# Optimization experiments

Hardware: AMD Instinct MI355X
Metric: run time of the kernel (lower is better)

## Reference

```python
import jax, jax.numpy as jnp
from jax import lax
import numpy as np

# dims
B, P, M = 256, 192, 321
HIDC, HIDR, HIDS = 128, 128, 8
CK, SKIP, HW = 6, 24, 24
SCI_K = 5
PT = (P - CK) // SKIP            # 7
NUM_LEVELS = 3
N_BLOCKS = 2 ** NUM_LEVELS - 1   # 7 Interactor blocks in the tree
PAD = (SCI_K - 1) // 2 + 1       # replication pad = 3 each side (odd kernel)


def setup_inputs() -> dict:
    key = jax.random.key(0)
    ks = jax.random.split(key, 18)
    s = 0.05
    def n(k, shape):
        return jax.random.normal(k, shape, jnp.float32) * s
    return {
        "x": jax.random.normal(ks[0], (B, P, M), jnp.float32),
        # SCINet tree params, stacked: [block, branch(phi,psi,U,P), ...]
        "tree_w1": n(ks[1], (N_BLOCKS, 4, M, M, SCI_K)),
        "tree_b1": n(ks[2], (N_BLOCKS, 4, M)),
        "tree_w2": n(ks[3], (N_BLOCKS, 4, M, M, 3)),
        "tree_b2": n(ks[4], (N_BLOCKS, 4, M)),
        "conv1_w": n(ks[5], (HIDC, 1, CK, M)),
        "conv1_b": n(ks[6], (HIDC,)),
        "gru1_wih": n(ks[7], (3 * HIDR, HIDC)),
        "gru1_whh": n(ks[8], (3 * HIDR, HIDR)),
        "gru1_bih": n(ks[9], (3 * HIDR,)),
        "gru1_bhh": n(ks[10], (3 * HIDR,)),
        "grus_wih": n(ks[11], (3 * HIDS, HIDC)),
        "grus_whh": n(ks[12], (3 * HIDS, HIDS)),
        "grus_bih": n(ks[13], (3 * HIDS,)),
        "grus_bhh": n(ks[14], (3 * HIDS,)),
        "lin1_w": n(ks[15], (M, HIDR + SKIP * HIDS)),
        "lin1_b": n(ks[16], (M,)),
        "hw_w": n(ks[17], (1, HW)),
        "hw_b": jnp.zeros((1,), jnp.float32),
    }


def _conv1d(z, w, b):
    # z: (B, Cin, T), w: (Cout, Cin, K) -> (B, Cout, T-K+1)
    y = lax.conv_general_dilated(z, w, (1,), 'VALID',
                                 dimension_numbers=('NCH', 'OIH', 'NCH'))
    return y + b[None, :, None]


def _gru_last(xs, wih, whh, bih, bhh, hidden):
    # xs: (T, N, I); returns final hidden (N, H). torch GRU gate order r,z,n.
    def step(h, xt):
        gi = xt @ wih.T + bih
        gh = h @ whh.T + bhh
        ir, iz, inn = jnp.split(gi, 3, -1)
        hr, hz, hn = jnp.split(gh, 3, -1)
        r = jax.nn.sigmoid(ir + hr)
        zt = jax.nn.sigmoid(iz + hz)
        nt = jnp.tanh(inn + r * hn)
        return (1.0 - zt) * nt + zt * h, None
    h0 = jnp.zeros((xs.shape[1], hidden), xs.dtype)
    hN, _ = lax.scan(step, h0, xs)
    return hN


def reference(x, tree_w1, tree_b1, tree_w2, tree_b2, conv1_w, conv1_b,
              gru1_wih, gru1_whh, gru1_bih, gru1_bhh,
              grus_wih, grus_whh, grus_bih, grus_bhh,
              lin1_w, lin1_b, hw_w, hw_b):
    def branch(z, i, j):
        # ReplicationPad -> Conv1d k=5 -> LeakyReLU(0.01) -> Conv1d k=3 -> Tanh
        zp = jnp.pad(z, ((0, 0), (0, 0), (PAD, PAD)), mode='edge')
        y = _conv1d(zp, tree_w1[i, j], tree_b1[i, j])
        y = jnp.where(y > 0, y, 0.01 * y)
        y = _conv1d(y, tree_w2[i, j], tree_b2[i, j])
        return jnp.tanh(y)

    counter = [0]
    def tree(z, level):
        # z: (B, T, M). Interactor (INN=True) then recurse / interleave.
        i = counter[0]; counter[0] += 1
        e = z[:, ::2, :].transpose(0, 2, 1)   # (B, M, T/2)
        o = z[:, 1::2, :].transpose(0, 2, 1)
        d = o * jnp.exp(branch(e, i, 0))      # phi
        c = e * jnp.exp(branch(o, i, 1))      # psi
        eu = (c + branch(d, i, 2)).transpose(0, 2, 1)  # U
        ou = (d - branch(c, i, 3)).transpose(0, 2, 1)  # P
        if level > 0:
            eu = tree(eu, level - 1)
            ou = tree(ou, level - 1)
        # zip_up_the_pants: even/odd lengths equal (T divisible by 2^levels)
        b_, l_, m_ = eu.shape
        return jnp.stack([eu, ou], axis=2).reshape(b_, 2 * l_, m_)

    res1 = tree(x, NUM_LEVELS - 1)
    xr = x + res1                              # (B, P, M)

    # Conv2d(1->hidC, kernel (Ck, m)) over (P, m), full-width kernel
    c = lax.conv_general_dilated(xr[:, None, :, :], conv1_w, (1, 1), 'VALID',
                                 dimension_numbers=('NCHW', 'OIHW', 'NCHW'))
    c = jax.nn.relu(c + conv1_b[None, :, None, None])[:, :, :, 0]  # (B,HIDC,L)

    # GRU1 over time
    r = _gru_last(c.transpose(2, 0, 1), gru1_wih, gru1_whh, gru1_bih, gru1_bhh, HIDR)

    # skip GRU
    s = c[:, :, -PT * SKIP:].reshape(B, HIDC, PT, SKIP)
    s = s.transpose(2, 0, 3, 1).reshape(PT, B * SKIP, HIDC)
    s = _gru_last(s, grus_wih, grus_whh, grus_bih, grus_bhh, HIDS)
    s = s.reshape(B, SKIP * HIDS)

    r = jnp.concatenate([r, s], axis=1)
    res = r @ lin1_w.T + lin1_b                # (B, M)

    # highway: AR component over last hw steps per series
    z = xr[:, -HW:, :].transpose(0, 2, 1).reshape(-1, HW)
    z = (z @ hw_w.T + hw_b).reshape(-1, M)
    return res + z
```

## Files before the change

### kernel.cpp

```cpp
#include <hip/hip_runtime.h>
#include <cstddef>
#include <cstdint>

#define Bn 256
#define Pn 192
#define Mn 321
#define Mp 336
#define HIDCn 128
#define HIDRn 128
#define HIDSn 8
#define CKn 6
#define SKIPn 24
#define HWn 24
#define Ln 187
#define PTn 7

typedef _Float16 f16;
typedef f16 f16x2 __attribute__((ext_vector_type(2)));
typedef f16 f16x8 __attribute__((ext_vector_type(8)));
typedef float f32x4 __attribute__((ext_vector_type(4)));
typedef float f32x16 __attribute__((ext_vector_type(16)));

__device__ __forceinline__ float sigmf(float x) { return 1.f / (1.f + expf(-x)); }

__device__ __forceinline__ void gll16(const void* g, void* l) {
#if defined(__has_builtin) && __has_builtin(__builtin_amdgcn_global_load_lds)
  __builtin_amdgcn_global_load_lds((const __attribute__((address_space(1))) void*)g,
                                   (__attribute__((address_space(3))) void*)l, 16, 0, 0);
#else
  *(uint4*)l = *(const uint4*)g;
#endif
}

__device__ __forceinline__ int lanepos(int co, int cc) {
  int ctg = co >> 5, row = co & 31;
  int h = (cc >> 3) & 1, d = (cc >> 1) & 3;
  return ((ctg * 256 + h * 128 + row * 4 + d) << 1) | (cc & 1);
}

__global__ __launch_bounds__(256) void repack_w(const float* __restrict__ w, f16* __restrict__ out,
                                                int K, int c0, int c1, int c2) {
  int s = blockIdx.z;
  int n = s >> 2, jj = s & 3;
  int blk = c0 + c1 * n + c2 * (n >> 1);
  int kcib = blockIdx.y;
  int k = kcib / 21, cib = kcib - 21 * k;
  int idx = blockIdx.x * 256 + threadIdx.x;
  int co = idx >> 4, cc = idx & 15;
  int ci = cib * 16 + cc;
  f16 val = (f16)0.f;
  if (co < Mn && ci < Mn)
    val = (f16)w[(((size_t)(blk * 4 + jj) * Mn + co) * Mn + ci) * K + k];
  out[(((size_t)s * K + k) * 21 + cib) * 6144 + lanepos(co, cc)] = val;
}

__global__ __launch_bounds__(256) void repack_c2w(const float* __restrict__ w, f16* __restrict__ out) {
  int idx = blockIdx.x * 256 + threadIdx.x;
  int cc = idx & 15;
  int co = (idx >> 4) & 127;
  int kcib = idx >> 11;
  int k = kcib / 21, cib = kcib - 21 * k;
  int m = cib * 16 + cc;
  f16 v = (f16)0.f;
  if (m < Mn) v = (f16)w[((size_t)co * CKn + k) * Mn + m];
  out[((size_t)(k * 21 + cib)) * 2048 + lanepos(co, cc)] = v;
}

__global__ __launch_bounds__(256) void deint_k(const float* __restrict__ x32,
                                               const f16* __restrict__ parent, int Thp,
                                               f16* __restrict__ o, int Th) {
  int b = blockIdx.x, t = blockIdx.y, z = blockIdx.z;
  int c = z >> 1, eo = z & 1;
  int srow = 2 * t + eo;
  size_t ooff = (((size_t)z * Bn + b) * Th + t) * Mp;
  if (x32) {
    const float* xp = x32 + ((size_t)b * Pn + srow) * Mn;
    for (int m = threadIdx.x; m < Mp; m += 256)
      o[ooff + m] = (m < Mn) ? (f16)xp[m] : (f16)0.f;
  } else {
    const uint32_t* ip = (const uint32_t*)(parent + (((size_t)c * Bn + b) * Thp + srow) * Mp);
    uint32_t* op = (uint32_t*)(o + ooff);
    for (int i = threadIdx.x; i < Mp / 2; i += 256) op[i] = ip[i];
  }
}

template <int K, int MK>
__global__ __launch_bounds__(512, 2) void conv_mfma(
    const f16* __restrict__ inz, long in_zs, int Tin,
    const f16* __restrict__ Wb, int wc0, int wc1, int wc2, int wjoff,
    const float* __restrict__ biasb,
    const f16* __restrict__ srcz, long src_zs,
    f16* __restrict__ outz, long out_zs, int Tout) {
  constexpr int PADL = (K == 5) ? 3 : 0;
  constexpr int TWIN = 32 + K - 1;
  constexpr int SLAB = K * 21 * 6144;
  constexpr int NS = 21 * K;
  __shared__ __align__(16) f16 sXs[2][4][40][24];
  __shared__ __align__(16) f16 sWs[2][6144];
  int z = blockIdx.z;
  int nnode = z >> 1, j = z & 1;
  int blk = wc0 + wc1 * nnode + wc2 * (nnode >> 1);
  int slot = nnode * 4 + wjoff + j;
  const uint4* inq = (const uint4*)(inz + (size_t)z * in_zs);
  const uint32_t* wsl = (const uint32_t*)(Wb + (size_t)slot * SLAB);
  const float* bias = biasb + (size_t)(blk * 4 + wjoff + j) * Mn;
  int b0 = blockIdx.x * 4;
  int t0 = blockIdx.y * 32;
  int tid = threadIdx.x;
  int lane = tid & 63;
  int wv = tid >> 6;
  int wm = wv & 3, wc = wv >> 2;

  f32x16 acc[6];
#pragma unroll
  for (int i = 0; i < 6; ++i)
#pragma unroll
    for (int q = 0; q < 16; ++q) acc[i][q] = 0.f;

  auto stageX = [&](int cib, int xb) {
    uint32_t* dXu = (uint32_t*)&sXs[xb][0][0][0];
    constexpr int NX4 = 4 * TWIN * 2;
    for (int idx = tid; idx < NX4; idx += 512) {
      int u2 = idx & 1;
      int rr = idx >> 1;
      int tt = rr % TWIN;
      int bl = rr / TWIN;
      int ts = t0 + tt - PADL;
      ts = max(0, min(ts, Tin - 1));
      uint4 v = inq[((((size_t)(b0 + bl)) * Tin + ts) * Mp + cib * 16) / 8 + u2];
      *(uint4*)&dXu[(bl * 40 + tt) * 12 + u2 * 4] = v;
    }
  };
  auto stageW = [&](int s, int wb) {
    int cib = s / K, k = s - cib * K;
    const uint32_t* wp = wsl + ((size_t)(k * 21 + cib)) * 3072;
    uint32_t* dst = (uint32_t*)&sWs[wb][0];
    for (int i = tid; i < 768; i += 512) gll16(wp + i * 4, dst + i * 4);
  };

  stageX(0, 0);
  stageW(0, 0);
  __syncthreads();
  int wb = 0, xb = 0;
#pragma unroll 1
  for (int s = 0; s < NS; ++s) {
    int cib = s / K, k = s - cib * K;
    if (s + 1 < NS) stageW(s + 1, wb ^ 1);
    if (k == K - 1 && cib + 1 < 21) stageX(cib + 1, xb ^ 1);
    f16x8 ah = *(const f16x8*)&sXs[xb][wm][(lane & 31) + k][(lane >> 5) * 8];
    const f16* sw = &sWs[wb][0];
#pragma unroll
    for (int ct = 0; ct < 6; ++ct) {
      f16x8 bw = *(const f16x8*)&sw[((wc * 6 + ct) * 256 + (lane >> 5) * 128 + (lane & 31) * 4) * 2];
      acc[ct] = __builtin_amdgcn_mfma_f32_32x32x16_f16(ah, bw, acc[ct], 0, 0, 0);
    }
    __syncthreads();
    wb ^= 1;
    if (k == K - 1) xb ^= 1;
  }
  f16* o = outz + (size_t)z * out_zs;
  const f16* s = srcz ? srcz + (size_t)(z ^ 1) * src_zs : nullptr;
#pragma unroll
  for (int ct = 0; ct < 6; ++ct) {
    int co = wc * 192 + ct * 32 + (lane & 31);
    if (co >= Mp) continue;
    float bb = (co < Mn) ? bias[co] : 0.f;
#pragma unroll
    for (int r = 0; r < 16; ++r) {
      int row = (r & 3) + 8 * (r >> 2) + 4 * (lane >> 5);
      int t = t0 + row;
      if (t >= Tout) continue;
      size_t oo = (((size_t)(b0 + wm)) * Tout + t) * Mp + co;
      float res;
      if (co >= Mn) {
        res = 0.f;
      } else {
        float v = acc[ct][r] + bb;
        if constexpr (MK == 0) {
          res = v > 0.f ? v : 0.01f * v;
        } else {
          float sv = (float)s[oo];
          float th = tanhf(v);
          if constexpr (MK == 1) res = sv * expf(th);
          else res = (j == 0) ? sv + th : sv - th;
        }
      }
      o[oo] = (f16)res;
    }
  }
}

__global__ __launch_bounds__(256) void combine_k(const float* __restrict__ x, const f16* __restrict__ lv,
                                                 float* __restrict__ XR, f16* __restrict__ XRh) {
  int b = blockIdx.x, p = blockIdx.y;
  int c = ((p & 1) << 2) | (p & 2) | ((p >> 2) & 1);
  int row = p >> 3;
  size_t li = (((size_t)c * Bn + b) * 24 + row) * Mp;
  size_t xi = ((size_t)b * Pn + p) * Mn;
  size_t hi = ((size_t)b * Pn + p) * Mp;
  for (int m = threadIdx.x; m < Mp; m += 256) {
    if (m < Mn) {
      float v = x[xi + m] + (float)lv[li + m];
      XR[xi + m] = v;
      XRh[hi + m] = (f16)v;
    } else {
      XRh[hi + m] = (f16)0.f;
    }
  }
}

__global__ __launch_bounds__(256, 4) void conv2d_mfma(
    const f16* __restrict__ xh, const f16* __restrict__ Wh,
    const float* __restrict__ bias, float* __restrict__ out) {
  __shared__ __align__(16) f16 sXs[2][9][32][24];
  __shared__ __align__(16) f16 sWs[2][2048];
  int b0 = blockIdx.x * 32;
  int l0 = blockIdx.y * 4;
  int tid = threadIdx.x;
  int lane = tid & 63;
  int wv = tid >> 6;

  f32x16 acc[4];
#pragma unroll
  for (int i = 0; i < 4; ++i)
#pragma unroll
    for (int q = 0; q < 16; ++q) acc[i][q] = 0.f;

  const uint4* xq = (const uint4*)xh;

  auto stageX = [&](int cib, int xb) {
    uint32_t* dXu = (uint32_t*)&sXs[xb][0][0][0];
    for (int idx = tid; idx < 576; idx += 256) {
      int u = idx & 1;
      int rr = idx >> 1;
      int bb = rr & 31, tt = rr >> 5;
      int p = min(l0 + tt, Pn - 1);
      uint4 v = xq[((((size_t)(b0 + bb)) * Pn + p) * Mp + cib * 16) / 8 + u];
      *(uint4*)&dXu[(tt * 32 + bb) * 12 + u * 4] = v;
    }
  };
  auto stageW = [&](int s, int wb) {
    int cib = s / CKn, k = s - cib * CKn;
    const uint32_t* wp = (const uint32_t*)(Wh + ((size_t)(k * 21 + cib)) * 2048);
    uint32_t* dst = (uint32_t*)&sWs[wb][0];
    gll16(wp + tid * 4, dst + tid * 4);
  };

  stageX(0, 0);
  stageW(0, 0);
  __syncthreads();
  int wb = 0, xb = 0;
#pragma unroll 1
  for (int s = 0; s < 126; ++s) {
    int cib = s / CKn, k = s - cib * CKn;
    if (s + 1 < 126) stageW(s + 1, wb ^ 1);
    if (k == CKn - 1 && cib + 1 < 21) stageX(cib + 1, xb ^ 1);
    f16x8 ah = *(const f16x8*)&sXs[xb][wv + k][lane & 31][(lane >> 5) * 8];
    const f16* sw = &sWs[wb][0];
#pragma unroll
    for (int ct = 0; ct < 4; ++ct) {
      f16x8 bw = *(const f16x8*)&sw[(ct * 256 + (lane >> 5) * 128 + (lane & 31) * 4) * 2];
      acc[ct] = __builtin_amdgcn_mfma_f32_32x32x16_f16(ah, bw, acc[ct], 0, 0, 0);
    }
    __syncthreads();
    wb ^= 1;
    if (k == CKn - 1) xb ^= 1;
  }
  int l = l0 + wv;
  if (l < Ln) {
#pragma unroll
    for (int ct = 0; ct < 4; ++ct) {
      int co = ct * 32 + (lane & 31);
      float bb = bias[co];
#pragma unroll
      for (int r = 0; r < 16; ++r) {
        int brow = (r & 3) + 8 * (r >> 2) + 4 * (lane >> 5);
        float y = acc[ct][r] + bb;
        out[((size_t)l * Bn + (b0 + brow)) * HIDCn + co] = y > 0.f ? y : 0.f;
      }
    }
  }
}

__global__ __launch_bounds__(256) void gemm_gi(const float* __restrict__ A, const float* __restrict__ W,
                                               const float* __restrict__ bias, float* __restrict__ out) {
  __shared__ float sA[64][129];
  __shared__ float sB[64][129];
  int r0 = blockIdx.x * 64, c0 = blockIdx.y * 64;
  int tid = threadIdx.x;
  for (int idx = tid; idx < 64 * 128; idx += 256) {
    int r = idx >> 7, k = idx & 127;
    sA[r][k] = A[(size_t)(r0 + r) * 128 + k];
    sB[r][k] = W[(size_t)(c0 + r) * 128 + k];
  }
  __syncthreads();
  int tx = tid & 15, ty = tid >> 4;
  int rr = ty * 4, cc = tx * 4;
  float acc[4][4] = {};
  for (int k = 0; k < 128; ++k) {
    float a[4], bv[4];
#pragma unroll
    for (int u = 0; u < 4; ++u) a[u] = sA[rr + u][k];
#pragma unroll
    for (int v = 0; v < 4; ++v) bv[v] = sB[cc + v][k];
#pragma unroll
    for (int u = 0; u < 4; ++u)
#pragma unroll
      for (int v = 0; v < 4; ++v) acc[u][v] = fmaf(a[u], bv[v], acc[u][v]);
  }
#pragma unroll
  for (int u = 0; u < 4; ++u)
#pragma unroll
    for (int v = 0; v < 4; ++v)
      out[(size_t)(r0 + rr + u) * 384 + (c0 + cc + v)] = acc[u][v] + bias[c0 + cc + v];
}

__global__ __launch_bounds__(384) void gru1_k(const float* __restrict__ gi, const float* __restrict__ whh,
                                              const float* __restrict__ bhh, float* __restrict__ hout) {
  __shared__ __align__(16) uint32_t hp[64];
  __shared__ float ghb[384];
  int n = blockIdx.x;
  int tid = threadIdx.x;
  int w = tid >> 6, l = tid & 63;
  int colg = l & 15, kg = l >> 4;

  f16x8 wfr[4][4];
#pragma unroll
  for (int gt = 0; gt < 4; ++gt) {
    int g = (w * 4 + gt) * 16 + colg;
#pragma unroll
    for (int q = 0; q < 4; ++q) {
      const float4* s4 = (const float4*)(whh + (size_t)g * 128 + q * 32 + kg * 8);
      float4 lo = s4[0], hi = s4[1];
      f16x8 f;
      f[0] = (f16)lo.x; f[1] = (f16)lo.y; f[2] = (f16)lo.z; f[3] = (f16)lo.w;
      f[4] = (f16)hi.x; f[5] = (f16)hi.y; f[6] = (f16)hi.z; f[7] = (f16)hi.w;
      wfr[gt][q] = f;
    }
  }
  float hreg = 0.f;
  float bh_r = 0.f, bh_z = 0.f, bh_n = 0.f;
  if (tid < 128) { bh_r = bhh[tid]; bh_z = bhh[128 + tid]; bh_n = bhh[256 + tid]; }
  if (tid < 64) hp[tid] = 0u;
  float grv = 0.f, gzv = 0.f, gnv = 0.f;
  if (tid < 128) {
    const float* gp = gi + (size_t)n * 384;
    grv = gp[tid]; gzv = gp[128 + tid]; gnv = gp[256 + tid];
  }
  __syncthreads();
  for (int t = 0; t < Ln; ++t) {
    float nrv = 0.f, nzv = 0.f, nnv = 0.f;
    if (tid < 128 && t + 1 < Ln) {
      const float* gp = gi + ((size_t)(t + 1) * Bn + n) * 384;
      nrv = gp[tid]; nzv = gp[128 + tid]; nnv = gp[256 + tid];
    }
    f32x4 acc[4];
#pragma unroll
    for (int gt = 0; gt < 4; ++gt)
#pragma unroll
      for (int q = 0; q < 4; ++q) acc[gt][q] = 0.f;
#pragma unroll
    for (int q = 0; q < 4; ++q) {
      f16x8 af = __builtin_bit_cast(f16x8, *(const uint4*)&hp[q * 16 + kg * 4]);
#pragma unroll
      for (int gt = 0; gt < 4; ++gt)
        acc[gt] = __builtin_amdgcn_mfma_f32_16x16x32_f16(af, wfr[gt][q], acc[gt], 0, 0, 0);
    }
    if (l < 16) {
#pragma unroll
      for (int gt = 0; gt < 4; ++gt) ghb[(w * 4 + gt) * 16 + colg] = acc[gt][0];
    }
    __syncthreads();
    if (tid < 128) {
      float rg = sigmf(grv + bh_r + ghb[tid]);
      float zg = sigmf(gzv + bh_z + ghb[128 + tid]);
      float ng = tanhf(gnv + bh_n + rg * ghb[256 + tid]);
      float hnew = (1.f - zg) * ng + zg * hreg;
      hreg = hnew;
      float other = __shfl_xor(hnew, 1, 64);
      if (!(tid & 1)) {
        f16 a = (f16)hnew, bq = (f16)other;
        hp[tid >> 1] = (uint32_t)__builtin_bit_cast(unsigned short, a) |
                       ((uint32_t)__builtin_bit_cast(unsigned short, bq) << 16);
      }
    }
    __syncthreads();
    grv = nrv; gzv = nzv; gnv = nnv;
  }
  if (tid < 128) hout[(size_t)n * 128 + tid] = hreg;
}

__global__ __launch_bounds__(256) void gis_k(const float* __restrict__ cc, const float* __restrict__ wih,
                                             const float* __restrict__ bih, float* __restrict__ gi) {
  __shared__ float sx[24 * 128];
  int t = blockIdx.x, b = blockIdx.y;
  int tid = threadIdx.x;
  for (int idx = tid; idx < 24 * 128; idx += 256) {
    int sk = idx >> 7, i = idx & 127;
    int l = 19 + t * 24 + sk;
    sx[idx] = cc[((size_t)l * Bn + b) * HIDCn + i];
  }
  __syncthreads();
  for (int idx = tid; idx < 576; idx += 256) {
    int sk = idx / 24, g = idx - sk * 24;
    float a = bih[g];
    for (int i = 0; i < 128; ++i) a = fmaf(sx[sk * 128 + i], wih[g * 128 + i], a);
    gi[((size_t)t * (Bn * SKIPn) + b * 24 + sk) * 24 + g] = a;
  }
}

__global__ __launch_bounds__(256) void grus_k(const float* __restrict__ gi, const float* __restrict__ whh,
                                              const float* __restrict__ bhh, float* __restrict__ hout) {
  __shared__ float sw[24 * 8];
  __shared__ float sb[24];
  int tid = threadIdx.x;
  int n = blockIdx.x * 256 + tid;
  if (tid < 192) sw[tid] = whh[tid];
  if (tid < 24) sb[tid] = bhh[tid];
  __syncthreads();
  float h[8];
#pragma unroll
  for (int jj = 0; jj < 8; ++jj) h[jj] = 0.f;
  for (int t = 0; t < PTn; ++t) {
    const float* gir = gi + ((size_t)t * (Bn * SKIPn) + n) * 24;
    float gh[24];
#pragma unroll
    for (int g = 0; g < 24; ++g) {
      float a = sb[g];
#pragma unroll
      for (int jj = 0; jj < 8; ++jj) a = fmaf(sw[g * 8 + jj], h[jj], a);
      gh[g] = a;
    }
#pragma unroll
    for (int jj = 0; jj < 8; ++jj) {
      float rg = sigmf(gir[jj] + gh[jj]);
      float zg = sigmf(gir[8 + jj] + gh[8 + jj]);
      float ng = tanhf(gir[16 + jj] + rg * gh[16 + jj]);
      h[jj] = (1.f - zg) * ng + zg * h[jj];
    }
  }
#pragma unroll
  for (int jj = 0; jj < 8; ++jj) hout[(size_t)n * 8 + jj] = h[jj];
}

__global__ __launch_bounds__(384) void final_k(const float* __restrict__ h1, const float* __restrict__ hsb,
                                               const float* __restrict__ lw, const float* __restrict__ lb,
                                               const float* __restrict__ xr, const float* __restrict__ hww,
                                               const float* __restrict__ hwb, float* __restrict__ out) {
  __shared__ float sr[320];
  __shared__ float shw[24];
  int b = blockIdx.x;
  int tid = threadIdx.x;
  if (tid < 128) sr[tid] = h1[(size_t)b * 128 + tid];
  else if (tid < 320) sr[tid] = hsb[(size_t)b * 192 + (tid - 128)];
  if (tid >= 320 && tid < 344) shw[tid - 320] = hww[tid - 320];
  __syncthreads();
  int m = tid;
  if (m >= Mn) return;
  float a = lb[m];
  const float* wr = lw + (size_t)m * 320;
  for (int c = 0; c < 320; ++c) a = fmaf(sr[c], wr[c], a);
  float z = hwb[0];
  const float* xrr = xr + ((size_t)b * Pn + (Pn - HWn)) * Mn + m;
#pragma unroll
  for (int k = 0; k < HWn; ++k) z = fmaf(xrr[(size_t)k * Mn], shw[k], z);
  out[(size_t)b * Mn + m] = a + z;
}

extern "C" void kernel_launch(void* const* d_in, const int* in_sizes, int n_in,
                              void* d_out, int out_size, void* d_ws, size_t ws_size,
                              hipStream_t stream) {
  const float* x = (const float*)d_in[0];
  const float* tw1 = (const float*)d_in[1];
  const float* tb1 = (const float*)d_in[2];
  const float* tw2 = (const float*)d_in[3];
  const float* tb2 = (const float*)d_in[4];
  const float* c1w = (const float*)d_in[5];
  const float* c1b = (const float*)d_in[6];
  const float* g1wih = (const float*)d_in[7];
  const float* g1whh = (const float*)d_in[8];
  const float* g1bih = (const float*)d_in[9];
  const float* g1bhh = (const float*)d_in[10];
  const float* gswih = (const float*)d_in[11];
  const float* gswhh = (const float*)d_in[12];
  const float* gsbih = (const float*)d_in[13];
  const float* gsbhh = (const float*)d_in[14];
  const float* l1w = (const float*)d_in[15];
  const float* l1b = (const float*)d_in[16];
  const float* hww = (const float*)d_in[17];
  const float* hwb = (const float*)d_in[18];
  float* out = (float*)d_out;

  const size_t Ah = 17891328ull, Bh = 17891328ull, Ch = 17203200ull;
  f16* Aq = (f16*)d_ws;
  f16* Bq = Aq + Ah;
  f16* Cq = Bq + Bh;
  f16* Wl1 = Cq + Ch;
  f16* Wl2 = Wl1 + 10321920ull;
  f16* Wc2 = (f16*)(Wl2 + 6193152ull);
  float* giA = (float*)(Wl2 + 6193152ull) + 246528ull;
  float* h1 = giA + 18382848ull;
  float* hsb = h1 + (size_t)Bn * HIDRn;
  float* gis = hsb + (size_t)Bn * SKIPn * HIDSn;
  float* XR = (float*)Bq;
  float* Cc = (float*)Aq;
  f16* XRh = Wl1;

  f16* EO[3] = {Aq, Aq, Bq};
  f16* S1[3] = {Bq, Cq, Aq};
  f16* CD[3] = {Cq, Bq, Cq};
  f16* S3[3] = {Aq, Aq, Bq};
  f16* EU[3] = {Bq, Cq, Aq};
  const int WC0[3] = {0, 1, 2}, WC1[3] = {0, 3, 1}, WC2[3] = {0, 0, 1};

  repack_c2w<<<dim3(1008), 256, 0, stream>>>(c1w, Wc2);

  for (int L = 0; L < 3; ++L) {
    int NL = 1 << L;
    int Th = 96 >> L;
    int Z = 2 * NL;
    long zsEO = (long)Bn * Th * Mp;
    long zsS1 = (long)Bn * (Th + 2) * Mp;
    repack_w<<<dim3(24, 5 * 21, NL * 4), 256, 0, stream>>>(tw1, Wl1, 5, WC0[L], WC1[L], WC2[L]);
    repack_w<<<dim3(24, 3 * 21, NL * 4), 256, 0, stream>>>(tw2, Wl2, 3, WC0[L], WC1[L], WC2[L]);
    if (L == 0)
      deint_k<<<dim3(Bn, Th, 2), 256, 0, stream>>>(x, nullptr, 0, EO[0], Th);
    else
      deint_k<<<dim3(Bn, Th, Z), 256, 0, stream>>>(nullptr, EU[L - 1], 2 * Th, EO[L], Th);
    int ty1 = (Th + 2 + 31) / 32, ty2 = (Th + 31) / 32;
    conv_mfma<5, 0><<<dim3(64, ty1, Z), 512, 0, stream>>>(
        EO[L], zsEO, Th, Wl1, WC0[L], WC1[L], WC2[L], 0, tb1,
        nullptr, 0, S1[L], zsS1, Th + 2);
    conv_mfma<3, 1><<<dim3(64, ty2, Z), 512, 0, stream>>>(
        S1[L], zsS1, Th + 2, Wl2, WC0[L], WC1[L], WC2[L], 0, tb2,
        EO[L], zsEO, CD[L], zsEO, Th);
    conv_mfma<5, 0><<<dim3(64, ty1, Z), 512, 0, stream>>>(
        CD[L], zsEO, Th, Wl1, WC0[L], WC1[L], WC2[L], 2, tb1,
        nullptr, 0, S3[L], zsS1, Th + 2);
    conv_mfma<3, 2><<<dim3(64, ty2, Z), 512, 0, stream>>>(
        S3[L], zsS1, Th + 2, Wl2, WC0[L], WC1[L], WC2[L], 2, tb2,
        CD[L], zsEO, EU[L], zsEO, Th);
  }

  combine_k<<<dim3(Bn, Pn), 256, 0, stream>>>(x, EU[2], XR, XRh);

  conv2d_mfma<<<dim3(Bn / 32, (Ln + 3) / 4), 256, 0, stream>>>(XRh, Wc2, c1b, Cc);
  gemm_gi<<<dim3((Ln * Bn) / 64, 384 / 64), 256, 0, stream>>>(Cc, g1wih, g1bih, giA);
  gru1_k<<<dim3(Bn), 384, 0, stream>>>(giA, g1whh, g1bhh, h1);
  gis_k<<<dim3(PTn, Bn), 256, 0, stream>>>(Cc, gswih, gsbih, gis);
  grus_k<<<dim3((Bn * SKIPn) / 256), 256, 0, stream>>>(gis, gswhh, gsbhh, hsb);
  final_k<<<dim3(Bn), 384, 0, stream>>>(h1, hsb, l1w, l1b, XR, hww, hwb, out);
}
```

Before: 1.893 ms.

## Use MFMA for GRU input GEMM, store conv output in fp16, restructure GRU1 step

The conv2d output is now stored in fp16, which halves its traffic. The GRU input-projection GEMM moves from a scalar fp32 LDS kernel to an MFMA 32x32x16 kernel, with weights repacked into lane layout and double-buffered. GRU1 now uses 512 threads, so each wave computes all three gates for its own 16 columns directly in registers. This removes the shared gate buffer and one of the two barriers per step, and uses ping-pong hidden-state buffers with a two-step gi prefetch. In exchange, the GEMM inputs lose precision to fp16.

```diff
diff --git a/kernel.cpp b/kernel.cpp
--- a/kernel.cpp
+++ b/kernel.cpp
@@ -64,6 +64,14 @@
   f16 v = (f16)0.f;
   if (m < Mn) v = (f16)w[((size_t)co * CKn + k) * Mn + m];
   out[((size_t)(k * 21 + cib)) * 2048 + lanepos(co, cc)] = v;
+}
+
+__global__ __launch_bounds__(256) void repack_giw(const float* __restrict__ w, f16* __restrict__ out) {
+  int idx = blockIdx.x * 256 + threadIdx.x;
+  int cc = idx & 15;
+  int co = (idx >> 4) % 384;
+  int k = idx / (16 * 384);
+  out[(size_t)k * 6144 + lanepos(co, cc)] = (f16)w[(size_t)co * 128 + k * 16 + cc];
 }
 
 __global__ __launch_bounds__(256) void deint_k(const float* __restrict__ x32,
@@ -211,7 +219,7 @@
 
 __global__ __launch_bounds__(256, 4) void conv2d_mfma(
     const f16* __restrict__ xh, const f16* __restrict__ Wh,
-    const float* __restrict__ bias, float* __restrict__ out) {
+    const float* __restrict__ bias, f16* __restrict__ out) {
   __shared__ __align__(16) f16 sXs[2][9][32][24];
   __shared__ __align__(16) f16 sWs[2][2048];
   int b0 = blockIdx.x * 32;
@@ -276,121 +284,145 @@
       for (int r = 0; r < 16; ++r) {
         int brow = (r & 3) + 8 * (r >> 2) + 4 * (lane >> 5);
         float y = acc[ct][r] + bb;
-        out[((size_t)l * Bn + (b0 + brow)) * HIDCn + co] = y > 0.f ? y : 0.f;
+        out[((size_t)l * Bn + (b0 + brow)) * HIDCn + co] = (f16)(y > 0.f ? y : 0.f);
       }
     }
   }
 }
 
-__global__ __launch_bounds__(256) void gemm_gi(const float* __restrict__ A, const float* __restrict__ W,
-                                               const float* __restrict__ bias, float* __restrict__ out) {
-  __shared__ float sA[64][129];
-  __shared__ float sB[64][129];
-  int r0 = blockIdx.x * 64, c0 = blockIdx.y * 64;
-  int tid = threadIdx.x;
-  for (int idx = tid; idx < 64 * 128; idx += 256) {
-    int r = idx >> 7, k = idx & 127;
-    sA[r][k] = A[(size_t)(r0 + r) * 128 + k];
-    sB[r][k] = W[(size_t)(c0 + r) * 128 + k];
-  }
-  __syncthreads();
-  int tx = tid & 15, ty = tid >> 4;
-  int rr = ty * 4, cc = tx * 4;
-  float acc[4][4] = {};
-  for (int k = 0; k < 128; ++k) {
-    float a[4], bv[4];
-#pragma unroll
-    for (int u = 0; u < 4; ++u) a[u] = sA[rr + u][k];
-#pragma unroll
-    for (int v = 0; v < 4; ++v) bv[v] = sB[cc + v][k];
-#pragma unroll
-    for (int u = 0; u < 4; ++u)
-#pragma unroll
-      for (int v = 0; v < 4; ++v) acc[u][v] = fmaf(a[u], bv[v], acc[u][v]);
-  }
-#pragma unroll
-  for (int u = 0; u < 4; ++u)
-#pragma unroll
-    for (int v = 0; v < 4; ++v)
-      out[(size_t)(r0 + rr + u) * 384 + (c0 + cc + v)] = acc[u][v] + bias[c0 + cc + v];
-}
-
-__global__ __launch_bounds__(384) void gru1_k(const float* __restrict__ gi, const float* __restrict__ whh,
+__global__ __launch_bounds__(512, 2) void gemm_gi(const f16* __restrict__ A, const f16* __restrict__ Wb,
+                                                  const float* __restrict__ bias, float* __restrict__ out) {
+  __shared__ __align__(16) f16 sA[128][136];
+  __shared__ __align__(16) f16 sW[2][6144];
+  int r0 = blockIdx.x * 128;
+  int tid = threadIdx.x;
+  int lane = tid & 63;
+  int wv = tid >> 6;
+  int wm = wv & 3, wc = wv >> 2;
+
+  const uint4* aq = (const uint4*)(A + (size_t)r0 * 128);
+  for (int i = tid; i < 2048; i += 512) {
+    int row = i >> 4, u = i & 15;
+    *(uint4*)&sA[row][u * 8] = aq[i];
+  }
+  {
+    const uint32_t* wp = (const uint32_t*)Wb;
+    uint32_t* dst = (uint32_t*)&sW[0][0];
+    for (int i = tid; i < 768; i += 512) gll16(wp + i * 4, dst + i * 4);
+  }
+  __syncthreads();
+
+  f32x16 acc[6];
+#pragma unroll
+  for (int i = 0; i < 6; ++i)
+#pragma unroll
+    for (int q = 0; q < 16; ++q) acc[i][q] = 0.f;
+
+  int wb = 0;
+#pragma unroll 1
+  for (int k = 0; k < 8; ++k) {
+    if (k + 1 < 8) {
+      const uint32_t* wp = (const uint32_t*)(Wb + (size_t)(k + 1) * 6144);
+      uint32_t* dst = (uint32_t*)&sW[wb ^ 1][0];
+      for (int i = tid; i < 768; i += 512) gll16(wp + i * 4, dst + i * 4);
+    }
+    f16x8 ah = *(const f16x8*)&sA[wm * 32 + (lane & 31)][k * 16 + (lane >> 5) * 8];
+    const f16* sw = &sW[wb][0];
+#pragma unroll
+    for (int ct = 0; ct < 6; ++ct) {
+      f16x8 bw = *(const f16x8*)&sw[((wc * 6 + ct) * 256 + (lane >> 5) * 128 + (lane & 31) * 4) * 2];
+      acc[ct] = __builtin_amdgcn_mfma_f32_32x32x16_f16(ah, bw, acc[ct], 0, 0, 0);
+    }
+    __syncthreads();
+    wb ^= 1;
+  }
+#pragma unroll
+  for (int ct = 0; ct < 6; ++ct) {
+    int c = wc * 192 + ct * 32 + (lane & 31);
+    float bb = bias[c];
+#pragma unroll
+    for (int r = 0; r < 16; ++r) {
+      int row = r0 + wm * 32 + (r & 3) + 8 * (r >> 2) + 4 * (lane >> 5);
+      out[(size_t)row * 384 + c] = acc[ct][r] + bb;
+    }
+  }
+}
+
+__global__ __launch_bounds__(512) void gru1_k(const float* __restrict__ gi, const float* __restrict__ whh,
                                               const float* __restrict__ bhh, float* __restrict__ hout) {
-  __shared__ __align__(16) uint32_t hp[64];
-  __shared__ float ghb[384];
+  __shared__ __align__(16) uint32_t hp[2][64];
   int n = blockIdx.x;
   int tid = threadIdx.x;
   int w = tid >> 6, l = tid & 63;
   int colg = l & 15, kg = l >> 4;
-
-  f16x8 wfr[4][4];
-#pragma unroll
-  for (int gt = 0; gt < 4; ++gt) {
-    int g = (w * 4 + gt) * 16 + colg;
+  int col = w * 16 + colg;
+
+  f16x8 wfr[3][4];
+#pragma unroll
+  for (int g = 0; g < 3; ++g) {
+    const float* wr = whh + (size_t)(g * 128 + col) * 128;
 #pragma unroll
     for (int q = 0; q < 4; ++q) {
-      const float4* s4 = (const float4*)(whh + (size_t)g * 128 + q * 32 + kg * 8);
+      const float4* s4 = (const float4*)(wr + q * 32 + kg * 8);
       float4 lo = s4[0], hi = s4[1];
       f16x8 f;
       f[0] = (f16)lo.x; f[1] = (f16)lo.y; f[2] = (f16)lo.z; f[3] = (f16)lo.w;
       f[4] = (f16)hi.x; f[5] = (f16)hi.y; f[6] = (f16)hi.z; f[7] = (f16)hi.w;
-      wfr[gt][q] = f;
-    }
-  }
-  float hreg = 0.f;
-  float bh_r = 0.f, bh_z = 0.f, bh_n = 0.f;
-  if (tid < 128) { bh_r = bhh[tid]; bh_z = bhh[128 + tid]; bh_n = bhh[256 + tid]; }
-  if (tid < 64) hp[tid] = 0u;
-  float grv = 0.f, gzv = 0.f, gnv = 0.f;
-  if (tid < 128) {
+      wfr[g][q] = f;
+    }
+  }
+  float bh_r = bhh[col], bh_z = bhh[128 + col], bh_n = bhh[256 + col];
+  if (tid < 128) ((uint32_t*)hp)[tid] = 0u;
+  float hprev = 0.f;
+  float gA0, gA1, gA2, gB0, gB1, gB2;
+  {
     const float* gp = gi + (size_t)n * 384;
-    grv = gp[tid]; gzv = gp[128 + tid]; gnv = gp[256 + tid];
-  }
-  __syncthreads();
-  for (int t = 0; t < Ln; ++t) {
-    float nrv = 0.f, nzv = 0.f, nnv = 0.f;
-    if (tid < 128 && t + 1 < Ln) {
-      const float* gp = gi + ((size_t)(t + 1) * Bn + n) * 384;
-      nrv = gp[tid]; nzv = gp[128 + tid]; nnv = gp[256 + tid];
-    }
-    f32x4 acc[4];
-#pragma unroll
-    for (int gt = 0; gt < 4; ++gt)
-#pragma unroll
-      for (int q = 0; q < 4; ++q) acc[gt][q] = 0.f;
+    gA0 = gp[col]; gA1 = gp[128 + col]; gA2 = gp[256 + col];
+    const float* gq = gi + ((size_t)Bn + n) * 384;
+    gB0 = gq[col]; gB1 = gq[128 + col]; gB2 = gq[256 + col];
+  }
+  __syncthreads();
+
+  auto gstep = [&](int T, float& G0, float& G1, float& G2, int RB) {
+    float u0 = G0, u1 = G1, u2 = G2;
+    if (T + 2 < Ln) {
+      const float* gp = gi + ((size_t)(T + 2) * Bn + n) * 384;
+      G0 = gp[col]; G1 = gp[128 + col]; G2 = gp[256 + col];
+    }
+    f32x4 ac0{}, ac1{}, ac2{};
 #pragma unroll
     for (int q = 0; q < 4; ++q) {
-      f16x8 af = __builtin_bit_cast(f16x8, *(const uint4*)&hp[q * 16 + kg * 4]);
-#pragma unroll
-      for (int gt = 0; gt < 4; ++gt)
-        acc[gt] = __builtin_amdgcn_mfma_f32_16x16x32_f16(af, wfr[gt][q], acc[gt], 0, 0, 0);
-    }
-    if (l < 16) {
-#pragma unroll
-      for (int gt = 0; gt < 4; ++gt) ghb[(w * 4 + gt) * 16 + colg] = acc[gt][0];
-    }
-    __syncthreads();
-    if (tid < 128) {
-      float rg = sigmf(grv + bh_r + ghb[tid]);
-      float zg = sigmf(gzv + bh_z + ghb[128 + tid]);
-      float ng = tanhf(gnv + bh_n + rg * ghb[256 + tid]);
-      float hnew = (1.f - zg) * ng + zg * hreg;
-      hreg = hnew;
-      float other = __shfl_xor(hnew, 1, 64);
-      if (!(tid & 1)) {
-        f16 a = (f16)hnew, bq = (f16)other;
-        hp[tid >> 1] = (uint32_t)__builtin_bit_cast(unsigned short, a) |
-                       ((uint32_t)__builtin_bit_cast(unsigned short, bq) << 16);
-      }
-    }
-    __syncthreads();
-    grv = nrv; gzv = nzv; gnv = nnv;
-  }
-  if (tid < 128) hout[(size_t)n * 128 + tid] = hreg;
-}
-
-__global__ __launch_bounds__(256) void gis_k(const float* __restrict__ cc, const float* __restrict__ wih,
+      f16x8 af = __builtin_bit_cast(f16x8, *(const uint4*)&hp[RB][q * 16 + kg * 4]);
+      ac0 = __builtin_amdgcn_mfma_f32_16x16x32_f16(af, wfr[0][q], ac0, 0, 0, 0);
+      ac1 = __builtin_amdgcn_mfma_f32_16x16x32_f16(af, wfr[1][q], ac1, 0, 0, 0);
+      ac2 = __builtin_amdgcn_mfma_f32_16x16x32_f16(af, wfr[2][q], ac2, 0, 0, 0);
+    }
+    float rg = sigmf(u0 + bh_r + ac0[0]);
+    float zg = sigmf(u1 + bh_z + ac1[0]);
+    float ng = tanhf(u2 + bh_n + rg * ac2[0]);
+    float hnew = (1.f - zg) * ng + zg * hprev;
+    hprev = hnew;
+    float other = __shfl_xor(hnew, 1, 64);
+    if (l < 16 && !(l & 1)) {
+      f16 a = (f16)hnew, b2 = (f16)other;
+      hp[RB ^ 1][w * 8 + (l >> 1)] = (uint32_t)__builtin_bit_cast(unsigned short, a) |
+                                     ((uint32_t)__builtin_bit_cast(unsigned short, b2) << 16);
+    }
+    asm volatile("s_waitcnt lgkmcnt(0)" ::: "memory");
+    __builtin_amdgcn_s_barrier();
+    asm volatile("" ::: "memory");
+  };
+
+#pragma unroll 1
+  for (int t = 0; t + 1 < Ln; t += 2) {
+    gstep(t, gA0, gA1, gA2, 0);
+    gstep(t + 1, gB0, gB1, gB2, 1);
+  }
+  gstep(Ln - 1, gA0, gA1, gA2, 0);
+  if (l < 16) hout[(size_t)n * 128 + col] = hprev;
+}
+
+__global__ __launch_bounds__(256) void gis_k(const f16* __restrict__ cc, const float* __restrict__ wih,
                                              const float* __restrict__ bih, float* __restrict__ gi) {
   __shared__ float sx[24 * 128];
   int t = blockIdx.x, b = blockIdx.y;
@@ -398,7 +430,7 @@
   for (int idx = tid; idx < 24 * 128; idx += 256) {
     int sk = idx >> 7, i = idx & 127;
     int l = 19 + t * 24 + sk;
-    sx[idx] = cc[((size_t)l * Bn + b) * HIDCn + i];
+    sx[idx] = (float)cc[((size_t)l * Bn + b) * HIDCn + i];
   }
   __syncthreads();
   for (int idx = tid; idx < 576; idx += 256) {
@@ -498,12 +530,13 @@
   f16* Wl1 = Cq + Ch;
   f16* Wl2 = Wl1 + 10321920ull;
   f16* Wc2 = (f16*)(Wl2 + 6193152ull);
+  f16* Wgi = Wc2 + 258048ull;
   float* giA = (float*)(Wl2 + 6193152ull) + 246528ull;
   float* h1 = giA + 18382848ull;
   float* hsb = h1 + (size_t)Bn * HIDRn;
   float* gis = hsb + (size_t)Bn * SKIPn * HIDSn;
   float* XR = (float*)Bq;
-  float* Cc = (float*)Aq;
+  f16* Cch = Aq;
   f16* XRh = Wl1;
 
   f16* EO[3] = {Aq, Aq, Bq};
@@ -514,6 +547,7 @@
   const int WC0[3] = {0, 1, 2}, WC1[3] = {0, 3, 1}, WC2[3] = {0, 0, 1};
 
   repack_c2w<<<dim3(1008), 256, 0, stream>>>(c1w, Wc2);
+  repack_giw<<<dim3(192), 256, 0, stream>>>(g1wih, Wgi);
 
   for (int L = 0; L < 3; ++L) {
     int NL = 1 << L;
@@ -544,10 +578,10 @@
 
   combine_k<<<dim3(Bn, Pn), 256, 0, stream>>>(x, EU[2], XR, XRh);
 
-  conv2d_mfma<<<dim3(Bn / 32, (Ln + 3) / 4), 256, 0, stream>>>(XRh, Wc2, c1b, Cc);
-  gemm_gi<<<dim3((Ln * Bn) / 64, 384 / 64), 256, 0, stream>>>(Cc, g1wih, g1bih, giA);
-  gru1_k<<<dim3(Bn), 384, 0, stream>>>(giA, g1whh, g1bhh, h1);
-  gis_k<<<dim3(PTn, Bn), 256, 0, stream>>>(Cc, gswih, gsbih, gis);
+  conv2d_mfma<<<dim3(Bn / 32, (Ln + 3) / 4), 256, 0, stream>>>(XRh, Wc2, c1b, Cch);
+  gemm_gi<<<dim3((Ln * Bn) / 128), 512, 0, stream>>>(Cch, Wgi, g1bih, giA);
+  gru1_k<<<dim3(Bn), 512, 0, stream>>>(giA, g1whh, g1bhh, h1);
+  gis_k<<<dim3(PTn, Bn), 256, 0, stream>>>(Cch, gswih, gsbih, gis);
   grus_k<<<dim3((Bn * SKIPn) / 256), 256, 0, stream>>>(gis, gswhh, gsbhh, hsb);
   final_k<<<dim3(Bn), 384, 0, stream>>>(h1, hsb, l1w, l1b, XR, hww, hwb, out);
 }
```

After: 1.815 ms. 1.04x faster.
